# Kernel optimization log

Measured on AMD Instinct MI355X. Metric: run time of the kernel, lower is better.

## Reference

```python
import jax, jax.numpy as jnp
import numpy as np

V, E, HD, T = 32000, 100, 256, 17   # vocab, embed dim, lstm hidden (bidir total), tagset
B, S = 64, 1024
H = HD // 2                         # per-direction hidden


def setup_inputs() -> dict:
    key = jax.random.key(0)
    ks = jax.random.split(key, 16)
    p = lambda k, sh: (jax.random.normal(k, sh, jnp.float32) * 0.1)
    sentence = jax.random.randint(ks[0], (B, S), 0, V)
    mask = jnp.ones((B, S), dtype=bool)
    embed = p(ks[1], (V, E)).at[0].set(0.0)  # padding_idx=0
    inp = {
        "sentence": sentence,
        "mask": mask,
        "embed": embed,
        "w_ih_f": p(ks[2], (4 * H, E)), "w_hh_f": p(ks[3], (4 * H, H)),
        "b_ih_f": p(ks[4], (4 * H,)), "b_hh_f": p(ks[5], (4 * H,)),
        "w_ih_b": p(ks[6], (4 * H, E)), "w_hh_b": p(ks[7], (4 * H, H)),
        "b_ih_b": p(ks[8], (4 * H,)), "b_hh_b": p(ks[9], (4 * H,)),
        "fc_w": p(ks[10], (T, HD)), "fc_b": p(ks[11], (T,)),
        "start_trans": p(ks[12], (T,)),
        "end_trans": p(ks[13], (T,)),
        "trans": p(ks[14], (T, T)),
    }
    return inp


def _lstm_dir(xs, w_ih, w_hh, b_ih, b_hh):
    # xs: [S, B, E] -> hs: [S, B, H]. PyTorch gate order: i, f, g, o.
    xg = jnp.einsum('sbe,ge->sbg', xs, w_ih) + b_ih  # precompute input projections
    h0 = jnp.zeros((xs.shape[1], H), xs.dtype)
    def step(carry, xg_t):
        h, c = carry
        g = xg_t + h @ w_hh.T + b_hh
        i, f, gg, o = jnp.split(g, 4, axis=-1)
        c = jax.nn.sigmoid(f) * c + jax.nn.sigmoid(i) * jnp.tanh(gg)
        h = jax.nn.sigmoid(o) * jnp.tanh(c)
        return (h, c), h
    _, hs = jax.lax.scan(step, (h0, h0), xg)
    return hs


def _emissions(sentence, embed, w_ih_f, w_hh_f, b_ih_f, b_hh_f,
               w_ih_b, w_hh_b, b_ih_b, b_hh_b, fc_w, fc_b):
    x = embed[sentence]                      # [B, S, E] (dropout is identity in eval)
    xs = x.transpose(1, 0, 2)                # [S, B, E]
    hf = _lstm_dir(xs, w_ih_f, w_hh_f, b_ih_f, b_hh_f)
    hb = _lstm_dir(xs[::-1], w_ih_b, w_hh_b, b_ih_b, b_hh_b)[::-1]
    hcat = jnp.concatenate([hf, hb], axis=-1)            # [S, B, 2H]
    return jnp.einsum('sbh,th->sbt', hcat, fc_w) + fc_b  # [S, B, T]


def reference(sentence, mask, embed, w_ih_f, w_hh_f, b_ih_f, b_hh_f,
              w_ih_b, w_hh_b, b_ih_b, b_hh_b, fc_w, fc_b,
              start_trans, end_trans, trans):
    em = _emissions(sentence, embed, w_ih_f, w_hh_f, b_ih_f, b_hh_f,
                    w_ih_b, w_hh_b, b_ih_b, b_hh_b, fc_w, fc_b)  # [S, B, T]
    mk = mask.T  # [S, B]

    # Viterbi forward pass (max-plus recurrence over the tagset)
    score0 = start_trans + em[0]  # [B, T]
    def vstep(score, inp):
        emit_t, mask_t = inp
        ns = score[:, :, None] + trans[None] + emit_t[:, None, :]  # [B, T_prev, T_cur]
        best = ns.max(axis=1)
        idx = jnp.argmax(ns, axis=1)                                # [B, T]
        score = jnp.where(mask_t[:, None], best, score)
        return score, idx
    score, hist = jax.lax.scan(vstep, score0, (em[1:], mk[1:]))    # hist: [S-1, B, T]
    score = score + end_trans
    last_tag = jnp.argmax(score, axis=-1)                          # [B]

    # Backtrace (mask-aware: frozen past sequence end)
    def back(tag, inp):
        idx_t, mask_t = inp
        prev = jnp.take_along_axis(idx_t, tag[:, None], axis=1)[:, 0]
        tag = jnp.where(mask_t, prev, tag)
        return tag, tag
    _, ys = jax.lax.scan(back, last_tag, (hist, mk[1:]), reverse=True)  # [S-1, B]
    path = jnp.concatenate([ys, last_tag[None]], axis=0).T              # [B, S]
    return path
```

## Files before the change

kernel.cpp:

```cpp
#include <hip/hip_runtime.h>
#include <math.h>

#define S_LEN 1024
#define BATCH 64
#define EDIM  100
#define HDIM  128
#define G4    512
#define TAGS  17

typedef __attribute__((ext_vector_type(2))) float f32x2;
typedef __attribute__((ext_vector_type(4))) float f32x4;

__device__ __forceinline__ f32x2 pkfma(f32x2 a, f32x2 b, f32x2 c) {
    return __builtin_elementwise_fma(a, b, c);
}

template<int CTRL>
__device__ __forceinline__ float qperm(float x) {
    int i = __float_as_int(x);
    i = __builtin_amdgcn_update_dpp(0, i, CTRL, 0xF, 0xF, true);
    return __int_as_float(i);
}
#define QX1 qperm<0xB1>
#define QX2 qperm<0x4E>

__device__ __forceinline__ float fast_tanh_u(float x) {
    float e = __expf(-2.f * x);
    return fmaf(2.f, __builtin_amdgcn_rcpf(1.f + e), -1.f);
}

#define RDLANE(v, jj) __int_as_float(__builtin_amdgcn_readlane(__float_as_int(v), (jj)))

#define STEP_BARRIER() do {                                          \
    __builtin_amdgcn_sched_barrier(0);                               \
    asm volatile("s_waitcnt lgkmcnt(0)\n\ts_barrier" ::: "memory");  \
    __builtin_amdgcn_sched_barrier(0);                               \
} while (0)

__global__ __launch_bounds__(512, 1) void fused_scan_proj(
    const float* __restrict__ xgf_s, const float* __restrict__ xgb_s,
    const float* __restrict__ w_hh_f, const float* __restrict__ w_hh_b,
    float* __restrict__ hcat, float* __restrict__ h_state, float* __restrict__ c_state,
    int t0_scan, int clen, int nscan,
    const int* __restrict__ sentence, const float* __restrict__ embed,
    const float* __restrict__ w_ih_f, const float* __restrict__ b_ih_f, const float* __restrict__ b_hh_f,
    const float* __restrict__ w_ih_b, const float* __restrict__ b_ih_b, const float* __restrict__ b_hh_b,
    float* __restrict__ xgf_p, float* __restrict__ xgb_p, int t0_proj, int nproj_n,
    const float* __restrict__ fc_w, const float* __restrict__ fc_b,
    float* __restrict__ em, int fc_t0a, int fc_t0b)
{
    __shared__ __align__(16) float smem[24576];

    if ((int)blockIdx.x < nscan) {
        const int t     = threadIdx.x;
        const int gid   = t >> 2, q = t & 3;
        const int b     = blockIdx.x & 63;
        const int dir   = blockIdx.x >> 6;
        const int chain = blockIdx.x;

        const float* whh = dir ? w_hh_b : w_hh_f;
        f32x2 wl[4][8], wh[4][8];
#pragma unroll
        for (int g4 = 0; g4 < 4; ++g4) {
            const f32x4* wr = (const f32x4*)(whh + (g4 * HDIM + gid) * HDIM + q * 32);
#pragma unroll
            for (int i = 0; i < 8; ++i) {
                f32x4 v = wr[i];
                wl[g4][i] = v.xy;
                wh[g4][i] = v.zw;
            }
        }

        typedef float hl_t[4][36];
        hl_t* h_lds = (hl_t*)smem;
        float c_reg = 0.f;
        if (t0_scan == 0) {
            if (t < HDIM) h_lds[0][t >> 5][t & 31] = 0.f;
        } else {
            c_reg = c_state[chain * HDIM + gid];
            if (t < HDIM) h_lds[0][t >> 5][t & 31] = h_state[chain * HDIM + t];
        }
        __syncthreads();

        const float* xgp = (dir ? xgb_s : xgf_s) + (long)b * G4 + gid * 4;
        float4 z4; z4.x = z4.y = z4.z = z4.w = 0.f;
        float4 xgc = *(const float4*)xgp;
        float4 xgn = (clen > 1) ? *(const float4*)(xgp + (long)BATCH * G4) : z4;

        float* hc_base = hcat + (long)b * S_LEN * 256 + dir * HDIM + gid;
        float hv = 0.f;
        float hbuf[8];

        for (int sb = 0; sb < clen; sb += 8) {
#pragma unroll
            for (int k = 0; k < 8; ++k) {
                const int s = sb + k;
                float4 xg2 = z4;
                if (s + 2 < clen) xg2 = *(const float4*)(xgp + (long)(s + 2) * BATCH * G4);

                const int cur = k & 1;
                const float* hp = &h_lds[cur][q][0];
                f32x2 ac0 = {0.f, 0.f}, ac1 = {0.f, 0.f}, ac2 = {0.f, 0.f}, ac3 = {0.f, 0.f};
#pragma unroll
                for (int i = 0; i < 8; ++i) {
                    f32x4 h4 = *(const f32x4*)(hp + i * 4);
                    f32x2 hlo = h4.xy, hhi = h4.zw;
                    ac0 = pkfma(wl[0][i], hlo, ac0); ac0 = pkfma(wh[0][i], hhi, ac0);
                    ac1 = pkfma(wl[1][i], hlo, ac1); ac1 = pkfma(wh[1][i], hhi, ac1);
                    ac2 = pkfma(wl[2][i], hlo, ac2); ac2 = pkfma(wh[2][i], hhi, ac2);
                    ac3 = pkfma(wl[3][i], hlo, ac3); ac3 = pkfma(wh[3][i], hhi, ac3);
                }
                float a0 = ac0.x + ac0.y, a1 = ac1.x + ac1.y;
                float a2 = ac2.x + ac2.y, a3 = ac3.x + ac3.y;

                a0 += QX1(a0); a1 += QX1(a1); a2 += QX1(a2); a3 += QX1(a3);
                a0 += QX2(a0); a1 += QX2(a1); a2 += QX2(a2); a3 += QX2(a3);

                float av = (q == 0) ? a0 : (q == 1) ? a1 : (q == 2) ? a2 : a3;
                float xv = (q == 0) ? xgc.x : (q == 1) ? xgc.y : (q == 2) ? xgc.z : xgc.w;
                float pre = xv + av;
                float xin = (q == 2) ? 2.f * pre : pre;
                float e   = __expf(-xin);
                float sgm = __builtin_amdgcn_rcpf(1.f + e);
                float act = (q == 2) ? fmaf(2.f, sgm, -1.f) : sgm;
                float t1 = QX1(act);
                float t2 = QX2(act);
                float t3 = QX2(t1);
                float gi = (q == 0) ? act : (q == 1) ? t1 : (q == 2) ? t2 : t3;
                float gf = (q == 1) ? act : (q == 0) ? t1 : (q == 3) ? t2 : t3;
                float gg = (q == 2) ? act : (q == 3) ? t1 : (q == 0) ? t2 : t3;
                float go = (q == 3) ? act : (q == 2) ? t1 : (q == 1) ? t2 : t3;
                c_reg = gf * c_reg + gi * gg;
                hv = go * fast_tanh_u(c_reg);
                hbuf[k] = hv;

                if (q == 0) h_lds[cur ^ 1][gid >> 5][gid & 31] = hv;
                STEP_BARRIER();
                xgc = xgn; xgn = xg2;
            }
            if (q == 0) {
#pragma unroll
                for (int k = 0; k < 8; ++k) {
                    int tg = dir ? (S_LEN - 1 - (t0_scan + sb + k)) : (t0_scan + sb + k);
                    hc_base[(long)tg * 256] = hbuf[k];
                }
            }
        }

        if (q == 0) {
            c_state[chain * HDIM + gid] = c_reg;
            h_state[chain * HDIM + gid] = hv;
        }
    } else if ((int)blockIdx.x < nscan + nproj_n) {
        if (t0_proj < 0) return;
        const int pb   = blockIdx.x - nscan;
        const int tid  = threadIdx.x;
        const int row0 = pb * 16;

        float (*xf)[EDIM] = (float(*)[EDIM])smem;
        float (*xb)[EDIM] = (float(*)[EDIM])(smem + 1600);
        int* tok = (int*)(smem + 3200);

        if (tid < 32) {
            int r = tid & 15;
            int row = row0 + r;
            int s = row >> 6, b = row & 63;
            int tt = (tid < 16) ? (t0_proj + s) : (S_LEN - 1 - (t0_proj + s));
            tok[tid] = sentence[b * S_LEN + tt];
        }
        __syncthreads();
        for (int i = tid; i < 16 * EDIM; i += 512) {
            int r = i / EDIM, e = i - r * EDIM;
            xf[r][e] = embed[(long)tok[r] * EDIM + e];
            xb[r][e] = embed[(long)tok[16 + r] * EDIM + e];
        }
        __syncthreads();

        const float* wptr[2];
        float bias[2];
#pragma unroll
        for (int ci = 0; ci < 2; ++ci) {
            int c = tid + 512 * ci;
            if (c < G4) { wptr[ci] = w_ih_f + c * EDIM; bias[ci] = b_ih_f[c] + b_hh_f[c]; }
            else { int cb = c - G4; wptr[ci] = w_ih_b + cb * EDIM; bias[ci] = b_ih_b[cb] + b_hh_b[cb]; }
        }

        float acc[2][16];
#pragma unroll
        for (int ci = 0; ci < 2; ++ci)
#pragma unroll
            for (int r = 0; r < 16; ++r) acc[ci][r] = 0.f;

        for (int e = 0; e < EDIM; e += 4) {
            float4 w4[2];
#pragma unroll
            for (int ci = 0; ci < 2; ++ci) w4[ci] = *(const float4*)(wptr[ci] + e);
#pragma unroll
            for (int r = 0; r < 16; ++r) {
                float4 xvf = *(const float4*)&xf[r][e];
                float4 xvb = *(const float4*)&xb[r][e];
#pragma unroll
                for (int ci = 0; ci < 2; ++ci) {
                    float4 xv = (ci == 0) ? xvf : xvb;
                    acc[ci][r] = fmaf(w4[ci].x, xv.x, acc[ci][r]);
                    acc[ci][r] = fmaf(w4[ci].y, xv.y, acc[ci][r]);
                    acc[ci][r] = fmaf(w4[ci].z, xv.z, acc[ci][r]);
                    acc[ci][r] = fmaf(w4[ci].w, xv.w, acc[ci][r]);
                }
            }
        }

#pragma unroll
        for (int ci = 0; ci < 2; ++ci) {
            int c = tid + 512 * ci;
#pragma unroll
            for (int r = 0; r < 16; ++r) {
                int row = row0 + r;
                float v = acc[ci][r] + bias[ci];
                if (c < G4) xgf_p[(long)row * G4 + (c & 127) * 4 + (c >> 7)] = v;
                else { int cb = c - G4; xgb_p[(long)row * G4 + (cb & 127) * 4 + (cb >> 7)] = v; }
            }
        }
    } else {
        const int fcb0 = blockIdx.x - nscan - nproj_n;
        const int nfc1 = clen >> 1;
        int fb, ft0;
        if (fcb0 < nfc1) { fb = fcb0; ft0 = fc_t0a; }
        else             { fb = fcb0 - nfc1; ft0 = fc_t0b; }
        if (ft0 < 0) return;

        const int tid = threadIdx.x;
        float* w_lds = smem;
        float* part  = smem + TAGS * 256;

        for (int i = tid; i < TAGS * 256; i += 512) w_lds[i] = fc_w[i];
        __syncthreads();

        const int r = tid >> 2, p = tid & 3;
        const int idx0 = fb * 128 + r;
        const int b  = idx0 / clen;
        const int i0 = idx0 - b * clen;
        const long row = (long)b * S_LEN + ft0 + i0;
        const float* hrow = hcat + row * 256 + p * 64;

        float acc[TAGS];
#pragma unroll
        for (int tg = 0; tg < TAGS; ++tg) acc[tg] = 0.f;

        for (int e4 = 0; e4 < 16; ++e4) {
            float4 xv = *(const float4*)(hrow + e4 * 4);
            const float* wp = w_lds + p * 64 + e4 * 4;
#pragma unroll
            for (int tg = 0; tg < TAGS; ++tg) {
                acc[tg] = fmaf(xv.x, wp[tg * 256 + 0], acc[tg]);
                acc[tg] = fmaf(xv.y, wp[tg * 256 + 1], acc[tg]);
                acc[tg] = fmaf(xv.z, wp[tg * 256 + 2], acc[tg]);
                acc[tg] = fmaf(xv.w, wp[tg * 256 + 3], acc[tg]);
            }
        }
#pragma unroll
        for (int tg = 0; tg < TAGS; ++tg) part[(r * TAGS + tg) * 4 + p] = acc[tg];
        __syncthreads();

        for (int idx = tid; idx < 128 * TAGS; idx += 512) {
            int rr = idx / TAGS, tg = idx - rr * TAGS;
            const float* pp = part + (rr * TAGS + tg) * 4;
            float v = ((pp[0] + pp[1]) + (pp[2] + pp[3])) + fc_b[tg];
            int ridx = fb * 128 + rr;
            int bb = ridx / clen;
            int ii = ridx - bb * clen;
            em[((long)bb * S_LEN + ft0 + ii) * TAGS + tg] = v;
        }
    }
}

#define MAX3(a,b,c) fmaxf(fmaxf((a),(b)),(c))
#define MIN3(a,b,c) min(min((a),(b)),(c))

__device__ __forceinline__ float max17(const float* a) {
    float m0 = MAX3(a[0], a[1], a[2]);
    float m1 = MAX3(a[3], a[4], a[5]);
    float m2 = MAX3(a[6], a[7], a[8]);
    float m3 = MAX3(a[9], a[10], a[11]);
    float m4 = MAX3(a[12], a[13], a[14]);
    float m5 = fmaxf(a[15], a[16]);
    float n0 = MAX3(m0, m1, m2);
    float n1 = MAX3(m3, m4, m5);
    return fmaxf(n0, n1);
}

__global__ __launch_bounds__(256) void decode_kernel(
    const float* __restrict__ em,
    const float* __restrict__ start_trans, const float* __restrict__ end_trans,
    const float* __restrict__ trans, int* __restrict__ out)
{
    const int b = blockIdx.x;
    const int tid = threadIdx.x;
    __shared__ __align__(16) float e_lds[S_LEN * TAGS];
    __shared__ __align__(16) float s_lds[S_LEN * TAGS];
    __shared__ float s_tr[TAGS * TAGS];
    __shared__ unsigned char hist[S_LEN * TAGS];
    __shared__ int tags[S_LEN];
    __shared__ int lt;

    {
        const float4* ef4 = (const float4*)(em + (long)b * S_LEN * TAGS);
        float4* el4 = (float4*)e_lds;
        for (int i = tid; i < (S_LEN * TAGS) / 4; i += 256) el4[i] = ef4[i];
        for (int i = tid; i < TAGS * TAGS; i += 256) s_tr[i] = trans[i];
    }
    __syncthreads();

    if (tid < 64) {
        const int lane = tid;
        const int cl = (lane < TAGS) ? lane : 0;
        float tcol[TAGS], etr[TAGS];
#pragma unroll
        for (int jj = 0; jj < TAGS; ++jj) {
            tcol[jj] = s_tr[jj * TAGS + cl];
            etr[jj]  = end_trans[jj];
        }

        float sc = start_trans[cl] + e_lds[cl];
        if (lane < TAGS) s_lds[cl] = sc;

        float em_cur = e_lds[1 * TAGS + cl];
#pragma unroll 2
        for (int s = 1; s < S_LEN; ++s) {
            int sn = (s + 1 < S_LEN) ? (s + 1) : s;
            float em_next = e_lds[sn * TAGS + cl];

            float a[TAGS];
#pragma unroll
            for (int jj = 0; jj < TAGS; ++jj)
                a[jj] = RDLANE(sc, jj) + tcol[jj];

            float amax = max17(a);
            sc = amax + em_cur;
            if (lane < TAGS) s_lds[s * TAGS + cl] = sc;
            em_cur = em_next;
        }

        float ev[TAGS];
#pragma unroll
        for (int jj = 0; jj < TAGS; ++jj) ev[jj] = RDLANE(sc, jj) + etr[jj];
        float bestv = max17(ev);
        int c[17];
#pragma unroll
        for (int j = 0; j < 17; ++j) c[j] = (ev[j] == bestv) ? j : 255;
        int m0 = MIN3(c[0], c[1], c[2]);
        int m1 = MIN3(c[3], c[4], c[5]);
        int m2 = MIN3(c[6], c[7], c[8]);
        int m3 = MIN3(c[9], c[10], c[11]);
        int m4 = MIN3(c[12], c[13], c[14]);
        int m5 = min(c[15], c[16]);
        int bt = min(MIN3(m0, m1, m2), MIN3(m3, m4, m5));
        if (lane == 0) lt = bt;
    }
    __syncthreads();

    for (int idx = tid; idx < (S_LEN - 1) * TAGS; idx += 256) {
        int s = idx / TAGS + 1;
        int c = idx - (s - 1) * TAGS;
        const float* sprev = s_lds + (s - 1) * TAGS;
        float emv = e_lds[s * TAGS + c];
        float cur = s_lds[s * TAGS + c];
        int bi = 255;
#pragma unroll
        for (int j = TAGS - 1; j >= 0; --j) {
            float v = (sprev[j] + s_tr[j * TAGS + c]) + emv;
            if (v == cur) bi = j;
        }
        hist[s * TAGS + c] = (unsigned char)bi;
    }
    __syncthreads();

    if (tid == 0) {
        int tag = lt;
        tags[S_LEN - 1] = tag;
        for (int s = S_LEN - 2; s >= 0; --s) {
            tag = hist[(s + 1) * TAGS + tag];
            tags[s] = tag;
        }
    }
    __syncthreads();
    for (int t = tid; t < S_LEN; t += 256) out[b * S_LEN + t] = tags[t];
}

extern "C" void kernel_launch(void* const* d_in, const int* in_sizes, int n_in,
                              void* d_out, int out_size, void* d_ws, size_t ws_size,
                              hipStream_t stream) {
    const int*   sentence    = (const int*)d_in[0];
    const float* embed       = (const float*)d_in[2];
    const float* w_ih_f      = (const float*)d_in[3];
    const float* w_hh_f      = (const float*)d_in[4];
    const float* b_ih_f      = (const float*)d_in[5];
    const float* b_hh_f      = (const float*)d_in[6];
    const float* w_ih_b      = (const float*)d_in[7];
    const float* w_hh_b      = (const float*)d_in[8];
    const float* b_ih_b      = (const float*)d_in[9];
    const float* b_hh_b      = (const float*)d_in[10];
    const float* fc_w        = (const float*)d_in[11];
    const float* fc_b        = (const float*)d_in[12];
    const float* start_trans = (const float*)d_in[13];
    const float* end_trans   = (const float*)d_in[14];
    const float* trans       = (const float*)d_in[15];
    int* out = (int*)d_out;

    const size_t hcat_e = (size_t)S_LEN * BATCH * 256;
    const size_t em_e   = (size_t)S_LEN * BATCH * TAGS;
    const size_t st_e   = (size_t)128 * HDIM;
    const size_t fixed  = hcat_e + em_e + 2 * st_e + 64;
    static const int cands[] = {1024, 512, 256, 128, 64};
    int C = 64;
    for (int ci = 0; ci < 5; ++ci) {
        int nch = S_LEN / cands[ci];
        size_t nbuf = (nch == 1) ? 2 : 4;
        size_t need = (nbuf * (size_t)cands[ci] * BATCH * G4 + fixed) * 4;
        if (need <= ws_size) { C = cands[ci]; break; }
    }
    const int nchunk = S_LEN / C;
    const size_t xg1 = (size_t)C * BATCH * G4;

    float* ws   = (float*)d_ws;
    float* xgf0 = ws;
    float* xgb0 = xgf0 + xg1;
    float* xgf1 = xgb0 + xg1;
    float* xgb1 = (nchunk > 1) ? xgf1 + xg1 : xgb0;
    float* base = (nchunk > 1) ? xgb1 + xg1 : xgf1;
    float* hcat     = base;
    float* em       = hcat + hcat_e;
    float* h_state  = em + em_e;
    float* c_state  = h_state + st_e;

    const int nproj = C * 4;
    const int nfc1  = C / 2;

    fused_scan_proj<<<nproj, 512, 0, stream>>>(
        nullptr, nullptr, w_hh_f, w_hh_b, hcat, h_state, c_state, 0, C, 0,
        sentence, embed, w_ih_f, b_ih_f, b_hh_f, w_ih_b, b_ih_b, b_hh_b,
        xgf0, xgb0, 0, nproj, fc_w, fc_b, em, -1, -1);

    for (int k = 0; k < nchunk; ++k) {
        const bool par1 = (k & 1) != 0;
        float* sf  = par1 ? xgf1 : xgf0;
        float* sbx = par1 ? xgb1 : xgb0;
        float* pf  = par1 ? xgf0 : xgf1;
        float* pbx = par1 ? xgb0 : xgb1;
        const bool hp = (k + 1 < nchunk);
        const int np = hp ? nproj : 0;

        int fca = -1, fcb = -1, nr = 0;
        if (2 * k >= nchunk + 1) {
            int m1 = k - 1, m2 = nchunk - k;
            fca = m1 * C; nr = 1;
            if (m2 != m1) { fcb = m2 * C; nr = 2; }
        }
        const int grid = 128 + np + nr * nfc1;
        fused_scan_proj<<<grid, 512, 0, stream>>>(
            sf, sbx, w_hh_f, w_hh_b, hcat, h_state, c_state, k * C, C, 128,
            sentence, embed, w_ih_f, b_ih_f, b_hh_f, w_ih_b, b_ih_b, b_hh_b,
            pf, pbx, hp ? (k + 1) * C : -1, np,
            fc_w, fc_b, em, fca, fcb);
    }
    {
        int fca = (nchunk - 1) * C;
        int fcb = (nchunk > 1) ? 0 : -1;
        int nr  = (nchunk > 1) ? 2 : 1;
        fused_scan_proj<<<nr * nfc1, 512, 0, stream>>>(
            nullptr, nullptr, w_hh_f, w_hh_b, hcat, h_state, c_state, 0, C, 0,
            sentence, embed, w_ih_f, b_ih_f, b_hh_f, w_ih_b, b_ih_b, b_hh_b,
            nullptr, nullptr, -1, 0, fc_w, fc_b, em, fca, fcb);
    }

    decode_kernel<<<BATCH, 256, 0, stream>>>(
        em, start_trans, end_trans, trans, out);
}
```

Measured before the change: 1.073 ms.

## Halve block size so each scan thread computes two hidden units

```diff
diff --git a/kernel.cpp b/kernel.cpp
--- a/kernel.cpp
+++ b/kernel.cpp
@@ -37,7 +37,7 @@
     __builtin_amdgcn_sched_barrier(0);                               \
 } while (0)
 
-__global__ __launch_bounds__(512, 1) void fused_scan_proj(
+__global__ __launch_bounds__(256, 1) void fused_scan_proj(
     const float* __restrict__ xgf_s, const float* __restrict__ xgb_s,
     const float* __restrict__ w_hh_f, const float* __restrict__ w_hh_b,
     float* __restrict__ hcat, float* __restrict__ h_state, float* __restrict__ c_state,
@@ -54,102 +54,145 @@
     if ((int)blockIdx.x < nscan) {
         const int t     = threadIdx.x;
         const int gid   = t >> 2, q = t & 3;
+        const int u0    = gid, u1 = gid + 64;
         const int b     = blockIdx.x & 63;
         const int dir   = blockIdx.x >> 6;
         const int chain = blockIdx.x;
 
         const float* whh = dir ? w_hh_b : w_hh_f;
-        f32x2 wl[4][8], wh[4][8];
+        f32x2 wl0[4][8], wh0[4][8], wl1[4][8], wh1[4][8];
 #pragma unroll
         for (int g4 = 0; g4 < 4; ++g4) {
-            const f32x4* wr = (const f32x4*)(whh + (g4 * HDIM + gid) * HDIM + q * 32);
+            const f32x4* wr0 = (const f32x4*)(whh + (g4 * HDIM + u0) * HDIM + q * 32);
+            const f32x4* wr1 = (const f32x4*)(whh + (g4 * HDIM + u1) * HDIM + q * 32);
 #pragma unroll
             for (int i = 0; i < 8; ++i) {
-                f32x4 v = wr[i];
-                wl[g4][i] = v.xy;
-                wh[g4][i] = v.zw;
+                f32x4 v0 = wr0[i];
+                wl0[g4][i] = v0.xy; wh0[g4][i] = v0.zw;
+                f32x4 v1 = wr1[i];
+                wl1[g4][i] = v1.xy; wh1[g4][i] = v1.zw;
             }
         }
 
         typedef float hl_t[4][36];
         hl_t* h_lds = (hl_t*)smem;
-        float c_reg = 0.f;
+        float c0 = 0.f, c1 = 0.f;
         if (t0_scan == 0) {
             if (t < HDIM) h_lds[0][t >> 5][t & 31] = 0.f;
         } else {
-            c_reg = c_state[chain * HDIM + gid];
+            c0 = c_state[chain * HDIM + u0];
+            c1 = c_state[chain * HDIM + u1];
             if (t < HDIM) h_lds[0][t >> 5][t & 31] = h_state[chain * HDIM + t];
         }
         __syncthreads();
 
-        const float* xgp = (dir ? xgb_s : xgf_s) + (long)b * G4 + gid * 4;
+        const float* xgbase = dir ? xgb_s : xgf_s;
+        const float* xgp0 = xgbase + (long)b * G4 + u0 * 4;
+        const float* xgp1 = xgbase + (long)b * G4 + u1 * 4;
         float4 z4; z4.x = z4.y = z4.z = z4.w = 0.f;
-        float4 xgc = *(const float4*)xgp;
-        float4 xgn = (clen > 1) ? *(const float4*)(xgp + (long)BATCH * G4) : z4;
-
-        float* hc_base = hcat + (long)b * S_LEN * 256 + dir * HDIM + gid;
-        float hv = 0.f;
-        float hbuf[8];
+        float4 xgc0 = *(const float4*)xgp0;
+        float4 xgc1 = *(const float4*)xgp1;
+        float4 xgn0 = (clen > 1) ? *(const float4*)(xgp0 + (long)BATCH * G4) : z4;
+        float4 xgn1 = (clen > 1) ? *(const float4*)(xgp1 + (long)BATCH * G4) : z4;
+
+        float* hcA = hcat + (long)b * S_LEN * 256 + dir * HDIM + u0;
+        float* hcB = hcat + (long)b * S_LEN * 256 + dir * HDIM + u1;
+        float hv0 = 0.f, hv1 = 0.f;
+        float hbufA[8], hbufB[8];
 
         for (int sb = 0; sb < clen; sb += 8) {
 #pragma unroll
             for (int k = 0; k < 8; ++k) {
                 const int s = sb + k;
-                float4 xg2 = z4;
-                if (s + 2 < clen) xg2 = *(const float4*)(xgp + (long)(s + 2) * BATCH * G4);
+                float4 xg20 = z4, xg21 = z4;
+                if (s + 2 < clen) {
+                    xg20 = *(const float4*)(xgp0 + (long)(s + 2) * BATCH * G4);
+                    xg21 = *(const float4*)(xgp1 + (long)(s + 2) * BATCH * G4);
+                }
 
                 const int cur = k & 1;
                 const float* hp = &h_lds[cur][q][0];
-                f32x2 ac0 = {0.f, 0.f}, ac1 = {0.f, 0.f}, ac2 = {0.f, 0.f}, ac3 = {0.f, 0.f};
+                f32x2 aA0 = {0.f,0.f}, aA1 = {0.f,0.f}, aA2 = {0.f,0.f}, aA3 = {0.f,0.f};
+                f32x2 aB0 = {0.f,0.f}, aB1 = {0.f,0.f}, aB2 = {0.f,0.f}, aB3 = {0.f,0.f};
 #pragma unroll
                 for (int i = 0; i < 8; ++i) {
                     f32x4 h4 = *(const f32x4*)(hp + i * 4);
                     f32x2 hlo = h4.xy, hhi = h4.zw;
-                    ac0 = pkfma(wl[0][i], hlo, ac0); ac0 = pkfma(wh[0][i], hhi, ac0);
-                    ac1 = pkfma(wl[1][i], hlo, ac1); ac1 = pkfma(wh[1][i], hhi, ac1);
-                    ac2 = pkfma(wl[2][i], hlo, ac2); ac2 = pkfma(wh[2][i], hhi, ac2);
-                    ac3 = pkfma(wl[3][i], hlo, ac3); ac3 = pkfma(wh[3][i], hhi, ac3);
+                    aA0 = pkfma(wl0[0][i], hlo, aA0); aA0 = pkfma(wh0[0][i], hhi, aA0);
+                    aA1 = pkfma(wl0[1][i], hlo, aA1); aA1 = pkfma(wh0[1][i], hhi, aA1);
+                    aA2 = pkfma(wl0[2][i], hlo, aA2); aA2 = pkfma(wh0[2][i], hhi, aA2);
+                    aA3 = pkfma(wl0[3][i], hlo, aA3); aA3 = pkfma(wh0[3][i], hhi, aA3);
+                    aB0 = pkfma(wl1[0][i], hlo, aB0); aB0 = pkfma(wh1[0][i], hhi, aB0);
+                    aB1 = pkfma(wl1[1][i], hlo, aB1); aB1 = pkfma(wh1[1][i], hhi, aB1);
+                    aB2 = pkfma(wl1[2][i], hlo, aB2); aB2 = pkfma(wh1[2][i], hhi, aB2);
+                    aB3 = pkfma(wl1[3][i], hlo, aB3); aB3 = pkfma(wh1[3][i], hhi, aB3);
                 }
-                float a0 = ac0.x + ac0.y, a1 = ac1.x + ac1.y;
-                float a2 = ac2.x + ac2.y, a3 = ac3.x + ac3.y;
-
-                a0 += QX1(a0); a1 += QX1(a1); a2 += QX1(a2); a3 += QX1(a3);
-                a0 += QX2(a0); a1 += QX2(a1); a2 += QX2(a2); a3 += QX2(a3);
-
-                float av = (q == 0) ? a0 : (q == 1) ? a1 : (q == 2) ? a2 : a3;
-                float xv = (q == 0) ? xgc.x : (q == 1) ? xgc.y : (q == 2) ? xgc.z : xgc.w;
-                float pre = xv + av;
-                float xin = (q == 2) ? 2.f * pre : pre;
-                float e   = __expf(-xin);
-                float sgm = __builtin_amdgcn_rcpf(1.f + e);
-                float act = (q == 2) ? fmaf(2.f, sgm, -1.f) : sgm;
-                float t1 = QX1(act);
-                float t2 = QX2(act);
-                float t3 = QX2(t1);
-                float gi = (q == 0) ? act : (q == 1) ? t1 : (q == 2) ? t2 : t3;
-                float gf = (q == 1) ? act : (q == 0) ? t1 : (q == 3) ? t2 : t3;
-                float gg = (q == 2) ? act : (q == 3) ? t1 : (q == 0) ? t2 : t3;
-                float go = (q == 3) ? act : (q == 2) ? t1 : (q == 1) ? t2 : t3;
-                c_reg = gf * c_reg + gi * gg;
-                hv = go * fast_tanh_u(c_reg);
-                hbuf[k] = hv;
-
-                if (q == 0) h_lds[cur ^ 1][gid >> 5][gid & 31] = hv;
+                float a0A = aA0.x + aA0.y, a1A = aA1.x + aA1.y;
+                float a2A = aA2.x + aA2.y, a3A = aA3.x + aA3.y;
+                float a0B = aB0.x + aB0.y, a1B = aB1.x + aB1.y;
+                float a2B = aB2.x + aB2.y, a3B = aB3.x + aB3.y;
+
+                a0A += QX1(a0A); a1A += QX1(a1A); a2A += QX1(a2A); a3A += QX1(a3A);
+                a0B += QX1(a0B); a1B += QX1(a1B); a2B += QX1(a2B); a3B += QX1(a3B);
+                a0A += QX2(a0A); a1A += QX2(a1A); a2A += QX2(a2A); a3A += QX2(a3A);
+                a0B += QX2(a0B); a1B += QX2(a1B); a2B += QX2(a2B); a3B += QX2(a3B);
+
+                float avA = (q == 0) ? a0A : (q == 1) ? a1A : (q == 2) ? a2A : a3A;
+                float avB = (q == 0) ? a0B : (q == 1) ? a1B : (q == 2) ? a2B : a3B;
+                float xvA = (q == 0) ? xgc0.x : (q == 1) ? xgc0.y : (q == 2) ? xgc0.z : xgc0.w;
+                float xvB = (q == 0) ? xgc1.x : (q == 1) ? xgc1.y : (q == 2) ? xgc1.z : xgc1.w;
+                float preA = xvA + avA;
+                float preB = xvB + avB;
+                float xinA = (q == 2) ? 2.f * preA : preA;
+                float xinB = (q == 2) ? 2.f * preB : preB;
+                float eA   = __expf(-xinA);
+                float eB   = __expf(-xinB);
+                float sgA  = __builtin_amdgcn_rcpf(1.f + eA);
+                float sgB  = __builtin_amdgcn_rcpf(1.f + eB);
+                float actA = (q == 2) ? fmaf(2.f, sgA, -1.f) : sgA;
+                float actB = (q == 2) ? fmaf(2.f, sgB, -1.f) : sgB;
+
+                float t1A = QX1(actA), t1B = QX1(actB);
+                float t2A = QX2(actA), t2B = QX2(actB);
+                float t3A = QX2(t1A),  t3B = QX2(t1B);
+                float giA = (q == 0) ? actA : (q == 1) ? t1A : (q == 2) ? t2A : t3A;
+                float gfA = (q == 1) ? actA : (q == 0) ? t1A : (q == 3) ? t2A : t3A;
+                float ggA = (q == 2) ? actA : (q == 3) ? t1A : (q == 0) ? t2A : t3A;
+                float goA = (q == 3) ? actA : (q == 2) ? t1A : (q == 1) ? t2A : t3A;
+                float giB = (q == 0) ? actB : (q == 1) ? t1B : (q == 2) ? t2B : t3B;
+                float gfB = (q == 1) ? actB : (q == 0) ? t1B : (q == 3) ? t2B : t3B;
+                float ggB = (q == 2) ? actB : (q == 3) ? t1B : (q == 0) ? t2B : t3B;
+                float goB = (q == 3) ? actB : (q == 2) ? t1B : (q == 1) ? t2B : t3B;
+                c0 = gfA * c0 + giA * ggA;
+                c1 = gfB * c1 + giB * ggB;
+                hv0 = goA * fast_tanh_u(c0);
+                hv1 = goB * fast_tanh_u(c1);
+                hbufA[k] = hv0;
+                hbufB[k] = hv1;
+
+                if (q == 0) {
+                    h_lds[cur ^ 1][gid >> 5][gid & 31] = hv0;
+                    h_lds[cur ^ 1][2 + (gid >> 5)][gid & 31] = hv1;
+                }
                 STEP_BARRIER();
-                xgc = xgn; xgn = xg2;
+                xgc0 = xgn0; xgn0 = xg20;
+                xgc1 = xgn1; xgn1 = xg21;
             }
             if (q == 0) {
 #pragma unroll
                 for (int k = 0; k < 8; ++k) {
                     int tg = dir ? (S_LEN - 1 - (t0_scan + sb + k)) : (t0_scan + sb + k);
-                    hc_base[(long)tg * 256] = hbuf[k];
+                    hcA[(long)tg * 256] = hbufA[k];
+                    hcB[(long)tg * 256] = hbufB[k];
                 }
             }
         }
 
         if (q == 0) {
-            c_state[chain * HDIM + gid] = c_reg;
-            h_state[chain * HDIM + gid] = hv;
+            c_state[chain * HDIM + u0] = c0;
+            h_state[chain * HDIM + u0] = hv0;
+            c_state[chain * HDIM + u1] = c1;
+            h_state[chain * HDIM + u1] = hv1;
         }
     } else if ((int)blockIdx.x < nscan + nproj_n) {
         if (t0_proj < 0) return;
@@ -169,39 +212,39 @@
             tok[tid] = sentence[b * S_LEN + tt];
         }
         __syncthreads();
-        for (int i = tid; i < 16 * EDIM; i += 512) {
+        for (int i = tid; i < 16 * EDIM; i += 256) {
             int r = i / EDIM, e = i - r * EDIM;
             xf[r][e] = embed[(long)tok[r] * EDIM + e];
             xb[r][e] = embed[(long)tok[16 + r] * EDIM + e];
         }
         __syncthreads();
 
-        const float* wptr[2];
-        float bias[2];
-#pragma unroll
-        for (int ci = 0; ci < 2; ++ci) {
-            int c = tid + 512 * ci;
+        const float* wptr[4];
+        float bias[4];
+#pragma unroll
+        for (int ci = 0; ci < 4; ++ci) {
+            int c = tid + 256 * ci;
             if (c < G4) { wptr[ci] = w_ih_f + c * EDIM; bias[ci] = b_ih_f[c] + b_hh_f[c]; }
             else { int cb = c - G4; wptr[ci] = w_ih_b + cb * EDIM; bias[ci] = b_ih_b[cb] + b_hh_b[cb]; }
         }
 
-        float acc[2][16];
-#pragma unroll
-        for (int ci = 0; ci < 2; ++ci)
+        float acc[4][16];
+#pragma unroll
+        for (int ci = 0; ci < 4; ++ci)
 #pragma unroll
             for (int r = 0; r < 16; ++r) acc[ci][r] = 0.f;
 
         for (int e = 0; e < EDIM; e += 4) {
-            float4 w4[2];
-#pragma unroll
-            for (int ci = 0; ci < 2; ++ci) w4[ci] = *(const float4*)(wptr[ci] + e);
+            float4 w4[4];
+#pragma unroll
+            for (int ci = 0; ci < 4; ++ci) w4[ci] = *(const float4*)(wptr[ci] + e);
 #pragma unroll
             for (int r = 0; r < 16; ++r) {
                 float4 xvf = *(const float4*)&xf[r][e];
                 float4 xvb = *(const float4*)&xb[r][e];
 #pragma unroll
-                for (int ci = 0; ci < 2; ++ci) {
-                    float4 xv = (ci == 0) ? xvf : xvb;
+                for (int ci = 0; ci < 4; ++ci) {
+                    float4 xv = (ci < 2) ? xvf : xvb;
                     acc[ci][r] = fmaf(w4[ci].x, xv.x, acc[ci][r]);
                     acc[ci][r] = fmaf(w4[ci].y, xv.y, acc[ci][r]);
                     acc[ci][r] = fmaf(w4[ci].z, xv.z, acc[ci][r]);
@@ -211,8 +254,8 @@
         }
 
 #pragma unroll
-        for (int ci = 0; ci < 2; ++ci) {
-            int c = tid + 512 * ci;
+        for (int ci = 0; ci < 4; ++ci) {
+            int c = tid + 256 * ci;
 #pragma unroll
             for (int r = 0; r < 16; ++r) {
                 int row = row0 + r;
@@ -223,7 +266,7 @@
         }
     } else {
         const int fcb0 = blockIdx.x - nscan - nproj_n;
-        const int nfc1 = clen >> 1;
+        const int nfc1 = clen;
         int fb, ft0;
         if (fcb0 < nfc1) { fb = fcb0; ft0 = fc_t0a; }
         else             { fb = fcb0 - nfc1; ft0 = fc_t0b; }
@@ -233,11 +276,11 @@
         float* w_lds = smem;
         float* part  = smem + TAGS * 256;
 
-        for (int i = tid; i < TAGS * 256; i += 512) w_lds[i] = fc_w[i];
+        for (int i = tid; i < TAGS * 256; i += 256) w_lds[i] = fc_w[i];
         __syncthreads();
 
         const int r = tid >> 2, p = tid & 3;
-        const int idx0 = fb * 128 + r;
+        const int idx0 = fb * 64 + r;
         const int b  = idx0 / clen;
         const int i0 = idx0 - b * clen;
         const long row = (long)b * S_LEN + ft0 + i0;
@@ -262,11 +305,11 @@
         for (int tg = 0; tg < TAGS; ++tg) part[(r * TAGS + tg) * 4 + p] = acc[tg];
         __syncthreads();
 
-        for (int idx = tid; idx < 128 * TAGS; idx += 512) {
+        for (int idx = tid; idx < 64 * TAGS; idx += 256) {
             int rr = idx / TAGS, tg = idx - rr * TAGS;
             const float* pp = part + (rr * TAGS + tg) * 4;
             float v = ((pp[0] + pp[1]) + (pp[2] + pp[3])) + fc_b[tg];
-            int ridx = fb * 128 + rr;
+            int ridx = fb * 64 + rr;
             int bb = ridx / clen;
             int ii = ridx - bb * clen;
             em[((long)bb * S_LEN + ft0 + ii) * TAGS + tg] = v;
@@ -434,9 +477,9 @@
     float* c_state  = h_state + st_e;
 
     const int nproj = C * 4;
-    const int nfc1  = C / 2;
-
-    fused_scan_proj<<<nproj, 512, 0, stream>>>(
+    const int nfc1  = C;
+
+    fused_scan_proj<<<nproj, 256, 0, stream>>>(
         nullptr, nullptr, w_hh_f, w_hh_b, hcat, h_state, c_state, 0, C, 0,
         sentence, embed, w_ih_f, b_ih_f, b_hh_f, w_ih_b, b_ih_b, b_hh_b,
         xgf0, xgb0, 0, nproj, fc_w, fc_b, em, -1, -1);
@@ -457,7 +500,7 @@
             if (m2 != m1) { fcb = m2 * C; nr = 2; }
         }
         const int grid = 128 + np + nr * nfc1;
-        fused_scan_proj<<<grid, 512, 0, stream>>>(
+        fused_scan_proj<<<grid, 256, 0, stream>>>(
             sf, sbx, w_hh_f, w_hh_b, hcat, h_state, c_state, k * C, C, 128,
             sentence, embed, w_ih_f, b_ih_f, b_hh_f, w_ih_b, b_ih_b, b_hh_b,
             pf, pbx, hp ? (k + 1) * C : -1, np,
@@ -467,7 +510,7 @@
         int fca = (nchunk - 1) * C;
         int fcb = (nchunk > 1) ? 0 : -1;
         int nr  = (nchunk > 1) ? 2 : 1;
-        fused_scan_proj<<<nr * nfc1, 512, 0, stream>>>(
+        fused_scan_proj<<<nr * nfc1, 256, 0, stream>>>(
             nullptr, nullptr, w_hh_f, w_hh_b, hcat, h_state, c_state, 0, C, 0,
             sentence, embed, w_ih_f, b_ih_f, b_hh_f, w_ih_b, b_ih_b, b_hh_b,
             nullptr, nullptr, -1, 0, fc_w, fc_b, em, fca, fcb);
```

Measured after the change: 1.627 ms. 51.6% more time.
